# Kernel tuning notes

Measured on AMD Instinct MI355X. Metric: run time of the kernel, lower is better.

## Reference

```python
import jax, jax.numpy as jnp
import numpy as np

NUM_EMBEDDINGS = 8192
EMBEDDING_DIM = 512
COMMITMENT_COST = 0.25
EMA_DECAY = 0.99
EPS = 1e-5


def setup_inputs() -> dict:
    key = jax.random.key(0)
    k1, k2, k3, k4 = jax.random.split(key, 4)
    B = 32768
    z = jax.random.normal(k1, (B, EMBEDDING_DIM), dtype=jnp.float32)
    weight = jax.random.normal(k2, (NUM_EMBEDDINGS, EMBEDDING_DIM), dtype=jnp.float32)
    ema_cluster_size = jax.random.uniform(k3, (NUM_EMBEDDINGS,), dtype=jnp.float32)
    ema_dw = jax.random.normal(k4, (NUM_EMBEDDINGS, EMBEDDING_DIM), dtype=jnp.float32)
    return {"z": z, "weight": weight, "ema_cluster_size": ema_cluster_size, "ema_dw": ema_dw}


def reference(z, weight, ema_cluster_size, ema_dw):
    K = weight.shape[0]
    # Squared-L2 distances: (B, K) = |z|^2 + |e|^2 - 2 z e^T
    distances = (
        jnp.sum(z * z, axis=1, keepdims=True)
        + jnp.sum(weight * weight, axis=1)
        - 2.0 * (z @ weight.T)
    )
    indices = jnp.argmin(distances, axis=1)          # (B,)
    quantized_raw = weight[indices]                  # (B, D) gather

    # EMA codebook update (training-mode buffers; one-hot scatter-add == segment_sum)
    counts = jax.ops.segment_sum(jnp.ones(z.shape[0], dtype=z.dtype), indices, num_segments=K)
    dw = jax.ops.segment_sum(z, indices, num_segments=K)  # encodings.T @ z
    new_cluster_size = ema_cluster_size * EMA_DECAY + (1.0 - EMA_DECAY) * counts
    new_ema_dw = ema_dw * EMA_DECAY + (1.0 - EMA_DECAY) * dw
    n = jnp.sum(new_cluster_size)
    cluster_size = (new_cluster_size + EPS) / (n + K * EPS) * n
    new_weight = new_ema_dw / cluster_size[:, None]

    commitment_loss = COMMITMENT_COST * jnp.mean((z - jax.lax.stop_gradient(quantized_raw)) ** 2)
    quantized = z + jax.lax.stop_gradient(quantized_raw - z)  # straight-through
    return quantized, indices, commitment_loss, new_weight, new_cluster_size, new_ema_dw
```

## Files before the change

### kernel.cpp

```cpp
#include <hip/hip_runtime.h>

#define B_N 32768
#define D_N 512
#define K_N 8192
#define EMA 0.99f
#define ONE_M_EMA 0.01f
#define EPS_ 1e-5f
#define CCOST 0.25f

#define ZP_OFF 295936ull
#define WP_OFF 100959232ull
#define WS_NEED (WP_OFF + 25165824ull)
#define CNT_OFF    295936ull
#define OFFS_OFF   332800ull
#define CURS_OFF   365568ull
#define ROWL_OFF   398336ull
#define LPART_OFF  529408ull

typedef __attribute__((ext_vector_type(8))) short bf16x8;
typedef __attribute__((ext_vector_type(4))) float f32x4;

__global__ __launch_bounds__(256) void prep_kernel(const float* __restrict__ w,
                                                   const float* __restrict__ ecs,
                                                   float* __restrict__ wsq,
                                                   float* __restrict__ ncs_out) {
  int row  = blockIdx.x * 4 + (threadIdx.x >> 6);
  int lane = threadIdx.x & 63;
  const float* p = w + (size_t)row * D_N + lane * 8;
  float4 a = *(const float4*)p;
  float4 b = *(const float4*)(p + 4);
  float s = a.x*a.x + a.y*a.y + a.z*a.z + a.w*a.w
          + b.x*b.x + b.y*b.y + b.z*b.z + b.w*b.w;
  #pragma unroll
  for (int off = 32; off; off >>= 1) s += __shfl_down(s, off);
  if (lane == 0) wsq[row] = s;

  int gid = blockIdx.x * 256 + threadIdx.x;
  if (gid < K_N) ncs_out[gid] = EMA * ecs[gid];
}

__global__ __launch_bounds__(256) void prep_nedw(const float4* __restrict__ edw,
                                                 float4* __restrict__ nedw) {
  int i = blockIdx.x * 256 + threadIdx.x;
  float4 v = edw[i];
  v.x *= EMA; v.y *= EMA; v.z *= EMA; v.w *= EMA;
  nedw[i] = v;
}

__global__ __launch_bounds__(256) void split_pack(const float* __restrict__ x,
                                                  ushort* __restrict__ xp,
                                                  int R, int mode) {
  int g   = blockIdx.x * 256 + threadIdx.x;
  int row = g >> 6, c = g & 63;
  const float* src = x + (size_t)row * 512 + c * 8;
  float v[8];
  *(float4*)&v[0] = *(const float4*)&src[0];
  *(float4*)&v[4] = *(const float4*)&src[4];
  uint hw[4], lw[4];
  #pragma unroll
  for (int i = 0; i < 4; i++) {
    uint b0 = __float_as_uint(v[2*i]);
    uint b1 = __float_as_uint(v[2*i+1]);
    float r0 = v[2*i]   - __uint_as_float(b0 & 0xFFFF0000u);
    float r1 = v[2*i+1] - __uint_as_float(b1 & 0xFFFF0000u);
    hw[i] = (b0 >> 16) | (b1 & 0xFFFF0000u);
    lw[i] = (__float_as_uint(r0) >> 16) | (__float_as_uint(r1) & 0xFFFF0000u);
  }
  uint4 H = {hw[0], hw[1], hw[2], hw[3]};
  uint4 L = {lw[0], lw[1], lw[2], lw[3]};
  int si  = c >> 2;
  int p   = (c & 3) ^ ((row >> 1) & 3);
  size_t sstr = (size_t)R * 32;
  size_t base = (size_t)row * 32 + (size_t)p * 8;
  size_t d0 = (size_t)(si)      * sstr + base;
  size_t d1 = (size_t)(16 + si) * sstr + base;
  size_t d2 = (size_t)(32 + si) * sstr + base;
  if (mode == 0) { *(uint4*)&xp[d0] = H; *(uint4*)&xp[d1] = H; *(uint4*)&xp[d2] = L; }
  else           { *(uint4*)&xp[d0] = H; *(uint4*)&xp[d1] = L; *(uint4*)&xp[d2] = H; }
}

constexpr int COLT2 = 8;

#define GLDS(SRC, DST) __builtin_amdgcn_global_load_lds((const unsigned int*)(SRC), (unsigned int*)(DST), 16, 0, 0)

#define PHASE(AC, BC, AL, BL, G)                                               \
  {                                                                            \
    const int g_ = (G);                                                        \
    if (g_ + 1 <= 383) {                                                       \
      const char* Ab_ = (const char*)As[(g_ + 1) & 3] + aoff;                  \
      const char* Bb_ = (const char*)Bs[(g_ + 1) & 3] + boff;                  \
      _Pragma("unroll")                                                        \
      for (int i_ = 0; i_ < 8; i_++) AL[i_] = *(const bf16x8*)(Ab_ + i_ * 1024);\
      _Pragma("unroll")                                                        \
      for (int j_ = 0; j_ < 4; j_++) BL[j_] = *(const bf16x8*)(Bb_ + j_ * 1024);\
    }                                                                          \
    if (g_ + 4 <= 383) {                                                       \
      const int slotF_ = sf & 3;                                               \
      GLDS(zA + (size_t)sf * 2097152,        (char*)As[slotF_] + t * 16);      \
      GLDS(zA + (size_t)sf * 2097152 + 8192, (char*)As[slotF_] + 8192 + t * 16);\
      const size_t wOfs_ = (size_t)sf * 524288 + (size_t)ctf * 16384;          \
      GLDS(wB + wOfs_,        (char*)Bs[slotF_] + t * 16);                     \
      GLDS(wB + wOfs_ + 8192, (char*)Bs[slotF_] + 8192 + t * 16);              \
      sf++; if (sf == 48) { sf = 0; ctf++; }                                   \
    }                                                                          \
    __builtin_amdgcn_s_setprio(1);                                             \
    _Pragma("unroll")                                                          \
    for (int i_ = 0; i_ < 8; i_++)                                             \
      _Pragma("unroll")                                                        \
      for (int j_ = 0; j_ < 4; j_++)                                           \
        acc[i_][j_] = __builtin_amdgcn_mfma_f32_16x16x32_bf16(AC[i_], BC[j_],  \
                                                        acc[i_][j_], 0, 0, 0); \
    __builtin_amdgcn_s_setprio(0);                                             \
    asm volatile("s_waitcnt lgkmcnt(0)" ::: "memory");                         \
    if (g_ <= 379)      { asm volatile("s_waitcnt vmcnt(8)" ::: "memory"); }   \
    else if (g_ == 380) { asm volatile("s_waitcnt vmcnt(4)" ::: "memory"); }   \
    else if (g_ == 381) { asm volatile("s_waitcnt vmcnt(0)" ::: "memory"); }   \
    __builtin_amdgcn_s_barrier();                                              \
    __builtin_amdgcn_sched_barrier(0);                                         \
  }

__global__ __launch_bounds__(512, 2) void score3p(
    const ushort* __restrict__ zp, const ushort* __restrict__ wp,
    const float* __restrict__ wsq, unsigned long long* __restrict__ packed) {
  __shared__ ushort As[4][8192];
  __shared__ ushort Bs[4][8192];
  __shared__ float wsqs[2048];
  __shared__ unsigned long long best2[256][4];

  const int t = threadIdx.x, lane = t & 63, wid = t >> 6;
  const int wm = wid >> 2, wn = wid & 3;
  const int l15 = lane & 15, lg = (lane >> 4) & 3;
  const int row0 = blockIdx.x * 256;
  const int cg0  = blockIdx.y * 2048;

  const char* zA = (const char*)zp + ((size_t)(row0 + (t >> 2)) * 64 + (size_t)(t & 3) * 16);
  const char* wB = (const char*)wp + ((size_t)(cg0  + (t >> 2)) * 64 + (size_t)(t & 3) * 16);

  const int swz  = (l15 >> 1) & 3;
  const int aoff = (wm * 128 + l15) * 64 + ((lg ^ swz) * 16);
  const int boff = (wn * 64  + l15) * 64 + ((lg ^ swz) * 16);

  { float4 v = *(const float4*)&wsq[cg0 + t * 4]; *(float4*)&wsqs[t * 4] = v; }
  if (t < 256) { best2[t][0] = ~0ull; best2[t][1] = ~0ull; best2[t][2] = ~0ull; best2[t][3] = ~0ull; }
  __syncthreads();

  #pragma unroll
  for (int s0 = 0; s0 < 4; s0++) {
    GLDS(zA + (size_t)s0 * 2097152,        (char*)As[s0] + t * 16);
    GLDS(zA + (size_t)s0 * 2097152 + 8192, (char*)As[s0] + 8192 + t * 16);
    GLDS(wB + (size_t)s0 * 524288,         (char*)Bs[s0] + t * 16);
    GLDS(wB + (size_t)s0 * 524288 + 8192,  (char*)Bs[s0] + 8192 + t * 16);
  }
  asm volatile("s_waitcnt vmcnt(8)" ::: "memory");
  __builtin_amdgcn_s_barrier();
  __builtin_amdgcn_sched_barrier(0);

  bf16x8 aE[8], bE[4], aO[8], bO[4];
  #pragma unroll
  for (int i = 0; i < 8; i++) aE[i] = *(const bf16x8*)((const char*)As[0] + aoff + i * 1024);
  #pragma unroll
  for (int j = 0; j < 4; j++) bE[j] = *(const bf16x8*)((const char*)Bs[0] + boff + j * 1024);
  asm volatile("s_waitcnt lgkmcnt(0)" ::: "memory");
  __builtin_amdgcn_s_barrier();
  __builtin_amdgcn_sched_barrier(0);

  int sf = 4, ctf = 0;

  for (int ct = 0; ct < COLT2; ct++) {
    f32x4 acc[8][4];
    #pragma unroll
    for (int i = 0; i < 8; i++)
      #pragma unroll
      for (int j = 0; j < 4; j++) acc[i][j] = (f32x4){0.f, 0.f, 0.f, 0.f};

    for (int s = 0; s < 48; s += 2) {
      const int g = ct * 48 + s;
      PHASE(aE, bE, aO, bO, g)
      PHASE(aO, bO, aE, bE, g + 1)
    }

    float rv[32]; int rx[32];
    #pragma unroll
    for (int i = 0; i < 8; i++)
      #pragma unroll
      for (int r = 0; r < 4; r++) {
        float bvv = 3.4e38f; int bii = 0;
        #pragma unroll
        for (int j = 0; j < 4; j++) {
          float wq = wsqs[ct * 256 + wn * 64 + j * 16 + l15];
          float dist = wq - 2.0f * acc[i][j][r];
          int c = cg0 + ct * 256 + wn * 64 + j * 16 + l15;
          if (dist < bvv) { bvv = dist; bii = c; }
        }
        rv[i * 4 + r] = bvv; rx[i * 4 + r] = bii;
      }
    #pragma unroll
    for (int e = 0; e < 32; e++) {
      float v = rv[e]; int ix = rx[e];
      #pragma unroll
      for (int m = 1; m < 16; m <<= 1) {
        float ov = __shfl_xor(v, m, 64);
        int   oi = __shfl_xor(ix, m, 64);
        if (ov < v || (ov == v && oi < ix)) { v = ov; ix = oi; }
      }
      rv[e] = v; rx[e] = ix;
    }
    #pragma unroll
    for (int half = 0; half < 2; half++) {
      const int e0 = l15 + half * 16;
      float bvv = 0.f; int bii = 0;
      #pragma unroll
      for (int e = 0; e < 32; e++) {
        bool p = (e == e0);
        bvv = p ? rv[e] : bvv; bii = p ? rx[e] : bii;
      }
      unsigned u = __float_as_uint(bvv);
      u = (u & 0x80000000u) ? ~u : (u | 0x80000000u);
      unsigned long long key = ((unsigned long long)u << 32) | (unsigned)bii;
      const int rowl = wm * 128 + (e0 >> 2) * 16 + lg * 4 + (e0 & 3);
      unsigned long long cur = best2[rowl][wn];
      if (key < cur) best2[rowl][wn] = key;
    }
  }

  __syncthreads();
  if (t < 256) {
    unsigned long long k0 = best2[t][0], k1 = best2[t][1];
    unsigned long long k2 = best2[t][2], k3 = best2[t][3];
    unsigned long long m0 = k0 < k1 ? k0 : k1;
    unsigned long long m1 = k2 < k3 ? k2 : k3;
    atomicMin(&packed[row0 + t], m0 < m1 ? m0 : m1);
  }
}

constexpr int LDP = 40;
constexpr int KSPLIT = 8, COLT = K_N / KSPLIT / 128;
__device__ __forceinline__ void stage16(const float* __restrict__ g,
                                        ushort* __restrict__ h,
                                        ushort* __restrict__ l) {
  float v[16];
  *(float4*)&v[0]  = *(const float4*)&g[0];
  *(float4*)&v[4]  = *(const float4*)&g[4];
  *(float4*)&v[8]  = *(const float4*)&g[8];
  *(float4*)&v[12] = *(const float4*)&g[12];
  uint hw[8], lw[8];
  #pragma unroll
  for (int i = 0; i < 8; i++) {
    uint b0 = __float_as_uint(v[2*i]);
    uint b1 = __float_as_uint(v[2*i+1]);
    float r0 = v[2*i]   - __uint_as_float(b0 & 0xFFFF0000u);
    float r1 = v[2*i+1] - __uint_as_float(b1 & 0xFFFF0000u);
    hw[i] = (b0 >> 16) | (b1 & 0xFFFF0000u);
    lw[i] = (__float_as_uint(r0) >> 16) | (__float_as_uint(r1) & 0xFFFF0000u);
  }
  ((uint4*)h)[0] = *(uint4*)&hw[0];
  ((uint4*)h)[1] = *(uint4*)&hw[4];
  ((uint4*)l)[0] = *(uint4*)&lw[0];
  ((uint4*)l)[1] = *(uint4*)&lw[4];
}

__global__ __launch_bounds__(256, 2) void score_argmin_mfma(
    const float* __restrict__ z, const float* __restrict__ w,
    const float* __restrict__ wsq, unsigned long long* __restrict__ packed) {
  __shared__ ushort Ah[128][LDP];
  __shared__ ushort Al[128][LDP];
  __shared__ ushort Bh[128][LDP];
  __shared__ ushort Bl[128][LDP];
  const int t = threadIdx.x, lane = t & 63, wid = t >> 6;
  const int wm = wid >> 1, wn = wid & 1;
  const int l15 = lane & 15, lg = lane >> 4;
  const int row0 = blockIdx.x * 128;
  const int ks0  = blockIdx.y * (K_N / KSPLIT);
  const int srow = t >> 1, skq = (t & 1) * 16;
  float rmin[16]; int ridx[16];
  #pragma unroll
  for (int e = 0; e < 16; e++) { rmin[e] = 3.4e38f; ridx[e] = 0; }
  for (int ct = 0; ct < COLT; ct++) {
    const int c0 = ks0 + ct * 128;
    f32x4 acc[4][4];
    #pragma unroll
    for (int i = 0; i < 4; i++)
      #pragma unroll
      for (int j = 0; j < 4; j++) acc[i][j] = (f32x4){0.f, 0.f, 0.f, 0.f};
    for (int k0 = 0; k0 < D_N; k0 += 32) {
      __syncthreads();
      stage16(&z[(size_t)(row0 + srow) * D_N + k0 + skq], &Ah[srow][skq], &Al[srow][skq]);
      stage16(&w[(size_t)(c0   + srow) * D_N + k0 + skq], &Bh[srow][skq], &Bl[srow][skq]);
      __syncthreads();
      bf16x8 ah[4], al[4], bh[4], bl[4];
      #pragma unroll
      for (int i = 0; i < 4; i++) {
        ah[i] = *(const bf16x8*)&Ah[wm*64 + i*16 + l15][lg*8];
        al[i] = *(const bf16x8*)&Al[wm*64 + i*16 + l15][lg*8];
        bh[i] = *(const bf16x8*)&Bh[wn*64 + i*16 + l15][lg*8];
        bl[i] = *(const bf16x8*)&Bl[wn*64 + i*16 + l15][lg*8];
      }
      #pragma unroll
      for (int i = 0; i < 4; i++)
        #pragma unroll
        for (int j = 0; j < 4; j++) {
          acc[i][j] = __builtin_amdgcn_mfma_f32_16x16x32_bf16(ah[i], bh[j], acc[i][j], 0, 0, 0);
          acc[i][j] = __builtin_amdgcn_mfma_f32_16x16x32_bf16(ah[i], bl[j], acc[i][j], 0, 0, 0);
          acc[i][j] = __builtin_amdgcn_mfma_f32_16x16x32_bf16(al[i], bh[j], acc[i][j], 0, 0, 0);
        }
    }
    float wq[4];
    #pragma unroll
    for (int j = 0; j < 4; j++) wq[j] = wsq[c0 + wn*64 + j*16 + l15];
    #pragma unroll
    for (int i = 0; i < 4; i++)
      #pragma unroll
      for (int r = 0; r < 4; r++) {
        const int e = i * 4 + r;
        #pragma unroll
        for (int j = 0; j < 4; j++) {
          float dist = wq[j] - 2.0f * acc[i][j][r];
          if (dist < rmin[e]) { rmin[e] = dist; ridx[e] = c0 + wn*64 + j*16 + l15; }
        }
      }
  }
  #pragma unroll
  for (int e = 0; e < 16; e++) {
    float v = rmin[e]; int ix = ridx[e];
    #pragma unroll
    for (int m = 1; m < 16; m <<= 1) {
      float ov = __shfl_xor(v, m, 64);
      int   oi = __shfl_xor(ix, m, 64);
      if (ov < v || (ov == v && oi < ix)) { v = ov; ix = oi; }
    }
    rmin[e] = v; ridx[e] = ix;
  }
  const int s = l15;
  float bv = 0.f; int bi = 0;
  #pragma unroll
  for (int e = 0; e < 16; e++) {
    bool p = (e == s);
    bv = p ? rmin[e] : bv;
    bi = p ? ridx[e] : bi;
  }
  unsigned u = __float_as_uint(bv);
  u = (u & 0x80000000u) ? ~u : (u | 0x80000000u);
  unsigned long long key = ((unsigned long long)u << 32) | (unsigned)bi;
  atomicMin(&packed[row0 + wm*64 + (s >> 2)*16 + lg*4 + (s & 3)], key);
}

__global__ __launch_bounds__(256) void count_kernel(
    const unsigned long long* __restrict__ packed, int* __restrict__ cnt,
    float* __restrict__ idxout) {
  int row = blockIdx.x * 256 + threadIdx.x;
  int idx = (int)(packed[row] & 0xFFFFFFFFull);
  idxout[row] = (float)idx;
  atomicAdd(&cnt[idx], 1);
}

__global__ __launch_bounds__(256) void scan_kernel(const int* __restrict__ cnt,
                                                   int* __restrict__ offs,
                                                   int* __restrict__ cursor) {
  int t = threadIdx.x;
  int base = t * 32;
  int local[32];
  int s = 0;
  #pragma unroll
  for (int i = 0; i < 32; i++) { local[i] = s; s += cnt[base + i]; }
  __shared__ int ps[257];
  ps[t + 1] = s;
  if (t == 0) ps[0] = 0;
  __syncthreads();
  if (t == 0) { for (int i = 1; i <= 256; i++) ps[i] += ps[i - 1]; }
  __syncthreads();
  int e = ps[t];
  #pragma unroll
  for (int i = 0; i < 32; i++) {
    int o = e + local[i];
    offs[base + i] = o; cursor[base + i] = o;
  }
  if (t == 255) offs[8192] = ps[256];
}

__global__ __launch_bounds__(256) void scatter_ids(
    const unsigned long long* __restrict__ packed, int* __restrict__ cursor,
    int* __restrict__ rowlist) {
  int row = blockIdx.x * 256 + threadIdx.x;
  int idx = (int)(packed[row] & 0xFFFFFFFFull);
  int pos = atomicAdd(&cursor[idx], 1);
  rowlist[pos] = row;
}

__global__ __launch_bounds__(256) void seg_accum(
    const float* __restrict__ z, const float* __restrict__ edw,
    const float* __restrict__ ecs, const int* __restrict__ offs,
    const int* __restrict__ rowlist, float* __restrict__ nedw_out,
    float* __restrict__ ncs_out) {
  int k = blockIdx.x, t = threadIdx.x;
  int s0 = offs[k], s1 = offs[k + 1];
  float ax = 0.f, ay = 0.f;
  for (int r = s0; r < s1; r++) {
    int row = rowlist[r];
    float2 zv = *(const float2*)&z[(size_t)row * D_N + t * 2];
    ax += zv.x; ay += zv.y;
  }
  float2 ev = *(const float2*)&edw[(size_t)k * D_N + t * 2];
  float2 o;
  o.x = EMA * ev.x + ONE_M_EMA * ax;
  o.y = EMA * ev.y + ONE_M_EMA * ay;
  *(float2*)&nedw_out[(size_t)k * D_N + t * 2] = o;
  if (t == 0) ncs_out[k] = EMA * ecs[k] + ONE_M_EMA * (float)(s1 - s0);
}

__global__ __launch_bounds__(256) void quant_loss(
    const float* __restrict__ z, const float* __restrict__ w,
    const unsigned long long* __restrict__ packed,
    float* __restrict__ qout, float* __restrict__ lpart) {
  int row = blockIdx.x, t = threadIdx.x;
  int idx = (int)(packed[row] & 0xFFFFFFFFull);
  float2 zv = *(const float2*)&z[(size_t)row * D_N + t * 2];
  float2 wv = *(const float2*)&w[(size_t)idx * D_N + t * 2];
  float2 q;
  q.x = zv.x + (wv.x - zv.x);
  q.y = zv.y + (wv.y - zv.y);
  *(float2*)&qout[(size_t)row * D_N + t * 2] = q;
  float dx = zv.x - wv.x, dy = zv.y - wv.y;
  float s = dx * dx + dy * dy;
  #pragma unroll
  for (int off = 32; off; off >>= 1) s += __shfl_down(s, off);
  __shared__ float part[4];
  if ((t & 63) == 0) part[t >> 6] = s;
  __syncthreads();
  if (t == 0) lpart[row] = part[0] + part[1] + part[2] + part[3];
}

__global__ __launch_bounds__(256) void reduce2(const float* __restrict__ ncs_out,
                                               const float* __restrict__ lpart,
                                               float* __restrict__ nsum,
                                               float* __restrict__ loss_sum) {
  int t = threadIdx.x;
  float s1 = 0.f, s2 = 0.f;
  for (int i = t; i < K_N; i += 256) s1 += ncs_out[i];
  for (int i = t; i < B_N; i += 256) s2 += lpart[i];
  #pragma unroll
  for (int off = 32; off; off >>= 1) {
    s1 += __shfl_down(s1, off);
    s2 += __shfl_down(s2, off);
  }
  __shared__ float p1[4], p2[4];
  if ((t & 63) == 0) { p1[t >> 6] = s1; p2[t >> 6] = s2; }
  __syncthreads();
  if (t == 0) {
    nsum[0]     = p1[0] + p1[1] + p1[2] + p1[3];
    loss_sum[0] = p2[0] + p2[1] + p2[2] + p2[3];
  }
}

__global__ __launch_bounds__(256) void gather_scatter(
    const float* __restrict__ z, const float* __restrict__ w,
    const unsigned long long* __restrict__ packed,
    float* __restrict__ qout, float* __restrict__ idxout,
    float* __restrict__ ncs_out, float* __restrict__ nedw_out,
    float* __restrict__ loss_sum) {
  int row = blockIdx.x;
  int t   = threadIdx.x;
  int idx = (int)(packed[row] & 0xFFFFFFFFull);
  float2 zv = *(const float2*)&z[(size_t)row * D_N + t * 2];
  float2 wv = *(const float2*)&w[(size_t)idx * D_N + t * 2];
  float2 q;
  q.x = zv.x + (wv.x - zv.x);
  q.y = zv.y + (wv.y - zv.y);
  *(float2*)&qout[(size_t)row * D_N + t * 2] = q;
  float dx = zv.x - wv.x, dy = zv.y - wv.y;
  float s = dx*dx + dy*dy;
  #pragma unroll
  for (int off = 32; off; off >>= 1) s += __shfl_down(s, off);
  __shared__ float part[4];
  if ((t & 63) == 0) part[t >> 6] = s;
  __syncthreads();
  if (t == 0) {
    atomicAdd(loss_sum, part[0] + part[1] + part[2] + part[3]);
    atomicAdd(&ncs_out[idx], ONE_M_EMA);
    idxout[row] = (float)idx;
  }
  atomicAdd(&nedw_out[(size_t)idx * D_N + t*2],     ONE_M_EMA * zv.x);
  atomicAdd(&nedw_out[(size_t)idx * D_N + t*2 + 1], ONE_M_EMA * zv.y);
}

__global__ __launch_bounds__(256) void reduce_n(const float* __restrict__ ncs_out,
                                                float* __restrict__ nsum) {
  int t = threadIdx.x;
  float s = 0.f;
  for (int i = t; i < K_N; i += 256) s += ncs_out[i];
  #pragma unroll
  for (int off = 32; off; off >>= 1) s += __shfl_down(s, off);
  __shared__ float part[4];
  if ((t & 63) == 0) part[t >> 6] = s;
  __syncthreads();
  if (t == 0) nsum[0] = part[0] + part[1] + part[2] + part[3];
}

__global__ __launch_bounds__(256) void finalize(
    const float* __restrict__ ncs_out, const float* __restrict__ nedw_out,
    float* __restrict__ nw_out, const float* __restrict__ nsum,
    const float* __restrict__ loss_sum, float* __restrict__ loss_out) {
  size_t i = (size_t)blockIdx.x * 256 + threadIdx.x;
  float n = nsum[0];
  int k = (int)(i >> 9);
  float nv = ncs_out[k];
  float cs = (nv + EPS_) / (n + K_N * EPS_) * n;
  nw_out[i] = nedw_out[i] / cs;
  if (i == 0) loss_out[0] = CCOST * loss_sum[0] / (float)((size_t)B_N * D_N);
}

extern "C" void kernel_launch(void* const* d_in, const int* in_sizes, int n_in,
                              void* d_out, int out_size, void* d_ws, size_t ws_size,
                              hipStream_t stream) {
  const float* z   = (const float*)d_in[0];
  const float* w   = (const float*)d_in[1];
  const float* ecs = (const float*)d_in[2];
  const float* edw = (const float*)d_in[3];

  float* out      = (float*)d_out;
  float* qout     = out;
  float* idxout   = out + (size_t)B_N * D_N;
  float* loss_out = idxout + B_N;
  float* nw_out   = loss_out + 1;
  float* ncs_out  = nw_out + (size_t)K_N * D_N;
  float* nedw_out = ncs_out + K_N;

  unsigned long long* packed = (unsigned long long*)d_ws;
  float* wsq      = (float*)((char*)d_ws + 262144);
  float* loss_sum = (float*)((char*)d_ws + 294912);
  float* nsum     = loss_sum + 1;

  hipMemsetAsync(d_ws, 0xFF, 262144, stream);
  hipMemsetAsync((void*)loss_sum, 0, 8, stream);

  prep_kernel<<<2048, 256, 0, stream>>>(w, ecs, wsq, ncs_out);

  if (ws_size >= WS_NEED) {
    ushort* zp  = (ushort*)((char*)d_ws + ZP_OFF);
    ushort* wp  = (ushort*)((char*)d_ws + WP_OFF);
    int* cnt    = (int*)((char*)d_ws + CNT_OFF);
    int* offs   = (int*)((char*)d_ws + OFFS_OFF);
    int* cursor = (int*)((char*)d_ws + CURS_OFF);
    int* rowl   = (int*)((char*)d_ws + ROWL_OFF);
    float* lpart= (float*)((char*)d_ws + LPART_OFF);

    split_pack<<<8192, 256, 0, stream>>>(z, zp, B_N, 0);
    split_pack<<<2048, 256, 0, stream>>>(w, wp, K_N, 1);
    score3p<<<dim3(128, 4), 512, 0, stream>>>(zp, wp, wsq, packed);
    hipMemsetAsync((void*)cnt, 0, K_N * sizeof(int), stream);
    count_kernel<<<B_N / 256, 256, 0, stream>>>(packed, cnt, idxout);
    scan_kernel<<<1, 256, 0, stream>>>(cnt, offs, cursor);
    scatter_ids<<<B_N / 256, 256, 0, stream>>>(packed, cursor, rowl);
    seg_accum<<<K_N, 256, 0, stream>>>(z, edw, ecs, offs, rowl, nedw_out, ncs_out);
    quant_loss<<<B_N, 256, 0, stream>>>(z, w, packed, qout, lpart);
    reduce2<<<1, 256, 0, stream>>>(ncs_out, lpart, nsum, loss_sum);
  } else {
    prep_nedw<<<4096, 256, 0, stream>>>((const float4*)edw, (float4*)nedw_out);
    score_argmin_mfma<<<dim3(B_N / 128, KSPLIT), 256, 0, stream>>>(z, w, wsq, packed);
    gather_scatter<<<B_N, 256, 0, stream>>>(z, w, packed, qout, idxout,
                                            ncs_out, nedw_out, loss_sum);
    reduce_n<<<1, 256, 0, stream>>>(ncs_out, nsum);
  }

  finalize<<<K_N * D_N / 256, 256, 0, stream>>>(ncs_out, nedw_out, nw_out,
                                                nsum, loss_sum, loss_out);
}
```

Measured before the change: 1.029 ms.

## Score with single bf16 pass and refine ambiguous rows with exact fp32 distances

Replaces the three-pass split-bf16 score GEMM (hi*hi, hi*lo, lo*hi) with a single hi*hi bf16 pass. Each tile keeps its best and second-best candidate, and a fixup kernel uses a Cauchy-Schwarz error bound on the dropped terms to accept rows whose winner is clearly separated. The remaining rows are queued and re-scored in fp32 over their candidate columns. This cuts GEMM work to about a third, at the cost of extra kernels, a large per-row candidate buffer, and refine work that depends on how many rows turn out ambiguous.

```diff
diff --git a/kernel.cpp b/kernel.cpp
--- a/kernel.cpp
+++ b/kernel.cpp
@@ -8,9 +8,14 @@
 #define EPS_ 1e-5f
 #define CCOST 0.25f
 
-#define ZP_OFF 295936ull
-#define WP_OFF 100959232ull
-#define WS_NEED (WP_OFF + 25165824ull)
+#define ZP_OFF    295936ull
+#define WP_OFF    33850368ull
+#define DIST_OFF  42238976ull
+#define THR_OFF   109347840ull
+#define ZH2_OFF   109478912ull
+#define ZL2_OFF   109609984ull
+#define QROWS_OFF 109741056ull
+#define WS_NEED   109872128ull
 #define CNT_OFF    295936ull
 #define OFFS_OFF   332800ull
 #define CURS_OFF   365568ull
@@ -47,36 +52,67 @@
   nedw[i] = v;
 }
 
-__global__ __launch_bounds__(256) void split_pack(const float* __restrict__ x,
-                                                  ushort* __restrict__ xp,
-                                                  int R, int mode) {
-  int g   = blockIdx.x * 256 + threadIdx.x;
+__global__ __launch_bounds__(256) void split_z(const float* __restrict__ x,
+                                               ushort* __restrict__ xp,
+                                               float* __restrict__ zh2,
+                                               float* __restrict__ zl2) {
+  int g = blockIdx.x * 256 + threadIdx.x;
   int row = g >> 6, c = g & 63;
   const float* src = x + (size_t)row * 512 + c * 8;
   float v[8];
   *(float4*)&v[0] = *(const float4*)&src[0];
   *(float4*)&v[4] = *(const float4*)&src[4];
-  uint hw[4], lw[4];
+  uint hw[4]; float h2 = 0.f, l2 = 0.f;
   #pragma unroll
   for (int i = 0; i < 4; i++) {
     uint b0 = __float_as_uint(v[2*i]);
     uint b1 = __float_as_uint(v[2*i+1]);
-    float r0 = v[2*i]   - __uint_as_float(b0 & 0xFFFF0000u);
-    float r1 = v[2*i+1] - __uint_as_float(b1 & 0xFFFF0000u);
+    float h0 = __uint_as_float(b0 & 0xFFFF0000u);
+    float h1 = __uint_as_float(b1 & 0xFFFF0000u);
+    float r0 = v[2*i] - h0, r1 = v[2*i+1] - h1;
     hw[i] = (b0 >> 16) | (b1 & 0xFFFF0000u);
-    lw[i] = (__float_as_uint(r0) >> 16) | (__float_as_uint(r1) & 0xFFFF0000u);
-  }
-  uint4 H = {hw[0], hw[1], hw[2], hw[3]};
-  uint4 L = {lw[0], lw[1], lw[2], lw[3]};
-  int si  = c >> 2;
-  int p   = (c & 3) ^ ((row >> 1) & 3);
-  size_t sstr = (size_t)R * 32;
-  size_t base = (size_t)row * 32 + (size_t)p * 8;
-  size_t d0 = (size_t)(si)      * sstr + base;
-  size_t d1 = (size_t)(16 + si) * sstr + base;
-  size_t d2 = (size_t)(32 + si) * sstr + base;
-  if (mode == 0) { *(uint4*)&xp[d0] = H; *(uint4*)&xp[d1] = H; *(uint4*)&xp[d2] = L; }
-  else           { *(uint4*)&xp[d0] = H; *(uint4*)&xp[d1] = L; *(uint4*)&xp[d2] = H; }
+    h2 += h0*h0 + h1*h1;  l2 += r0*r0 + r1*r1;
+  }
+  int si = c >> 2;
+  int p  = (c & 3) ^ ((row >> 1) & 3);
+  size_t d0 = (size_t)si * (32768u * 32u) + (size_t)row * 32 + (size_t)p * 8;
+  *(uint4*)&xp[d0] = (uint4){hw[0], hw[1], hw[2], hw[3]};
+  #pragma unroll
+  for (int off = 32; off; off >>= 1) { h2 += __shfl_down(h2, off); l2 += __shfl_down(l2, off); }
+  if (c == 0) { zh2[row] = h2; zl2[row] = l2; }
+}
+
+__global__ __launch_bounds__(256) void split_w(const float* __restrict__ x,
+                                               ushort* __restrict__ xp,
+                                               unsigned* __restrict__ maxwl2,
+                                               unsigned* __restrict__ maxw2) {
+  int g = blockIdx.x * 256 + threadIdx.x;
+  int row = g >> 6, c = g & 63;
+  const float* src = x + (size_t)row * 512 + c * 8;
+  float v[8];
+  *(float4*)&v[0] = *(const float4*)&src[0];
+  *(float4*)&v[4] = *(const float4*)&src[4];
+  uint hw[4]; float w2 = 0.f, l2 = 0.f;
+  #pragma unroll
+  for (int i = 0; i < 4; i++) {
+    uint b0 = __float_as_uint(v[2*i]);
+    uint b1 = __float_as_uint(v[2*i+1]);
+    float h0 = __uint_as_float(b0 & 0xFFFF0000u);
+    float h1 = __uint_as_float(b1 & 0xFFFF0000u);
+    float r0 = v[2*i] - h0, r1 = v[2*i+1] - h1;
+    hw[i] = (b0 >> 16) | (b1 & 0xFFFF0000u);
+    w2 += v[2*i]*v[2*i] + v[2*i+1]*v[2*i+1];  l2 += r0*r0 + r1*r1;
+  }
+  int si = c >> 2;
+  int p  = (c & 3) ^ ((row >> 1) & 3);
+  size_t d0 = (size_t)si * (8192u * 32u) + (size_t)row * 32 + (size_t)p * 8;
+  *(uint4*)&xp[d0] = (uint4){hw[0], hw[1], hw[2], hw[3]};
+  #pragma unroll
+  for (int off = 32; off; off >>= 1) { w2 += __shfl_down(w2, off); l2 += __shfl_down(l2, off); }
+  if (c == 0) {
+    atomicMax(maxwl2, __float_as_uint(l2));
+    atomicMax(maxw2,  __float_as_uint(w2));
+  }
 }
 
 constexpr int COLT2 = 8;
@@ -86,7 +122,7 @@
 #define PHASE(AC, BC, AL, BL, G)                                               \
   {                                                                            \
     const int g_ = (G);                                                        \
-    if (g_ + 1 <= 383) {                                                       \
+    if (g_ + 1 <= 127) {                                                       \
       const char* Ab_ = (const char*)As[(g_ + 1) & 3] + aoff;                  \
       const char* Bb_ = (const char*)Bs[(g_ + 1) & 3] + boff;                  \
       _Pragma("unroll")                                                        \
@@ -94,14 +130,14 @@
       _Pragma("unroll")                                                        \
       for (int j_ = 0; j_ < 4; j_++) BL[j_] = *(const bf16x8*)(Bb_ + j_ * 1024);\
     }                                                                          \
-    if (g_ + 4 <= 383) {                                                       \
+    if (g_ + 4 <= 127) {                                                       \
       const int slotF_ = sf & 3;                                               \
       GLDS(zA + (size_t)sf * 2097152,        (char*)As[slotF_] + t * 16);      \
       GLDS(zA + (size_t)sf * 2097152 + 8192, (char*)As[slotF_] + 8192 + t * 16);\
       const size_t wOfs_ = (size_t)sf * 524288 + (size_t)ctf * 16384;          \
       GLDS(wB + wOfs_,        (char*)Bs[slotF_] + t * 16);                     \
       GLDS(wB + wOfs_ + 8192, (char*)Bs[slotF_] + 8192 + t * 16);              \
-      sf++; if (sf == 48) { sf = 0; ctf++; }                                   \
+      sf++; if (sf == 16) { sf = 0; ctf++; }                                   \
     }                                                                          \
     __builtin_amdgcn_s_setprio(1);                                             \
     _Pragma("unroll")                                                          \
@@ -112,20 +148,19 @@
                                                         acc[i_][j_], 0, 0, 0); \
     __builtin_amdgcn_s_setprio(0);                                             \
     asm volatile("s_waitcnt lgkmcnt(0)" ::: "memory");                         \
-    if (g_ <= 379)      { asm volatile("s_waitcnt vmcnt(8)" ::: "memory"); }   \
-    else if (g_ == 380) { asm volatile("s_waitcnt vmcnt(4)" ::: "memory"); }   \
-    else if (g_ == 381) { asm volatile("s_waitcnt vmcnt(0)" ::: "memory"); }   \
+    if (g_ <= 123)      { asm volatile("s_waitcnt vmcnt(8)" ::: "memory"); }   \
+    else if (g_ == 124) { asm volatile("s_waitcnt vmcnt(4)" ::: "memory"); }   \
+    else if (g_ == 125) { asm volatile("s_waitcnt vmcnt(0)" ::: "memory"); }   \
     __builtin_amdgcn_s_barrier();                                              \
     __builtin_amdgcn_sched_barrier(0);                                         \
   }
 
-__global__ __launch_bounds__(512, 2) void score3p(
+__global__ __launch_bounds__(512, 2) void score_h(
     const ushort* __restrict__ zp, const ushort* __restrict__ wp,
-    const float* __restrict__ wsq, unsigned long long* __restrict__ packed) {
+    const float* __restrict__ wsq, float4* __restrict__ dist12) {
   __shared__ ushort As[4][8192];
   __shared__ ushort Bs[4][8192];
   __shared__ float wsqs[2048];
-  __shared__ unsigned long long best2[256][4];
 
   const int t = threadIdx.x, lane = t & 63, wid = t >> 6;
   const int wm = wid >> 2, wn = wid & 3;
@@ -141,7 +176,6 @@
   const int boff = (wn * 64  + l15) * 64 + ((lg ^ swz) * 16);
 
   { float4 v = *(const float4*)&wsq[cg0 + t * 4]; *(float4*)&wsqs[t * 4] = v; }
-  if (t < 256) { best2[t][0] = ~0ull; best2[t][1] = ~0ull; best2[t][2] = ~0ull; best2[t][3] = ~0ull; }
   __syncthreads();
 
   #pragma unroll
@@ -173,63 +207,157 @@
       #pragma unroll
       for (int j = 0; j < 4; j++) acc[i][j] = (f32x4){0.f, 0.f, 0.f, 0.f};
 
-    for (int s = 0; s < 48; s += 2) {
-      const int g = ct * 48 + s;
+    for (int s = 0; s < 16; s += 2) {
+      const int g = ct * 16 + s;
       PHASE(aE, bE, aO, bO, g)
       PHASE(aO, bO, aE, bE, g + 1)
     }
 
-    float rv[32]; int rx[32];
+    const int tileG = blockIdx.y * 8 + ct;
     #pragma unroll
-    for (int i = 0; i < 8; i++)
+    for (int ch = 0; ch < 4; ch++) {
+      float v1[8], v2[8]; int i1[8];
       #pragma unroll
-      for (int r = 0; r < 4; r++) {
-        float bvv = 3.4e38f; int bii = 0;
+      for (int u = 0; u < 8; u++) {
+        const int i = 2 * ch + (u >> 2), r = u & 3;
+        float b1 = 3.4e38f, b2 = 3.4e38f; int bi = 0x7FFFFFFF;
         #pragma unroll
         for (int j = 0; j < 4; j++) {
           float wq = wsqs[ct * 256 + wn * 64 + j * 16 + l15];
-          float dist = wq - 2.0f * acc[i][j][r];
-          int c = cg0 + ct * 256 + wn * 64 + j * 16 + l15;
-          if (dist < bvv) { bvv = dist; bii = c; }
+          float d  = wq - 2.0f * acc[i][j][r];
+          int cc   = cg0 + ct * 256 + wn * 64 + j * 16 + l15;
+          if (d < b1)      { b2 = b1; b1 = d; bi = cc; }
+          else if (d < b2) { b2 = d; }
         }
-        rv[i * 4 + r] = bvv; rx[i * 4 + r] = bii;
+        v1[u] = b1; i1[u] = bi; v2[u] = b2;
       }
-    #pragma unroll
-    for (int e = 0; e < 32; e++) {
-      float v = rv[e]; int ix = rx[e];
       #pragma unroll
-      for (int m = 1; m < 16; m <<= 1) {
-        float ov = __shfl_xor(v, m, 64);
-        int   oi = __shfl_xor(ix, m, 64);
-        if (ov < v || (ov == v && oi < ix)) { v = ov; ix = oi; }
+      for (int u = 0; u < 8; u++) {
+        float a1 = v1[u], a2 = v2[u]; int ai = i1[u];
+        #pragma unroll
+        for (int m = 1; m < 16; m <<= 1) {
+          float o1 = __shfl_xor(a1, m, 64);
+          int   oi = __shfl_xor(ai, m, 64);
+          float o2 = __shfl_xor(a2, m, 64);
+          bool tb = (o1 < a1) || (o1 == a1 && oi < ai);
+          float lose = tb ? a1 : o1;
+          a2 = fminf(fminf(a2, o2), lose);
+          a1 = tb ? o1 : a1; ai = tb ? oi : ai;
+        }
+        v1[u] = a1; i1[u] = ai; v2[u] = a2;
       }
-      rv[e] = v; rx[e] = ix;
+      const int wbase = (ch & 1) * 8;
+      if (l15 >= wbase && l15 < wbase + 8) {
+        const int eu = l15 - wbase;
+        float f1 = 0.f, f2 = 0.f; int fi = 0;
+        #pragma unroll
+        for (int u = 0; u < 8; u++) {
+          bool p = (u == eu);
+          f1 = p ? v1[u] : f1; fi = p ? i1[u] : fi; f2 = p ? v2[u] : f2;
+        }
+        const int e = 8 * ch + eu;
+        const int rowG = row0 + wm * 128 + (e >> 2) * 16 + lg * 4 + (e & 3);
+        float4 st; st.x = f1; st.y = __int_as_float(fi); st.z = f2; st.w = 0.f;
+        dist12[(size_t)rowG * 128 + tileG * 4 + wn] = st;
+      }
     }
+  }
+}
+
+__global__ __launch_bounds__(256) void fixup_kernel(
+    const float4* __restrict__ dist12, const float* __restrict__ zh2,
+    const float* __restrict__ zl2, const float* __restrict__ scal,
+    unsigned long long* __restrict__ packed, float* __restrict__ thresh_arr,
+    int* __restrict__ qrows, int* __restrict__ qcount) {
+  int row  = blockIdx.x * 4 + (threadIdx.x >> 6);
+  int lane = threadIdx.x & 63;
+  const float4* base = dist12 + (size_t)row * 128;
+  float4 ea = base[lane];
+  float4 eb = base[lane + 64];
+  float v1, v2; int i1;
+  {
+    bool tb = (eb.x < ea.x) || (eb.x == ea.x && __float_as_int(eb.y) < __float_as_int(ea.y));
+    float lose = tb ? ea.x : eb.x;
+    v2 = fminf(fminf(ea.z, eb.z), lose);
+    v1 = tb ? eb.x : ea.x;
+    i1 = __float_as_int(tb ? eb.y : ea.y);
+  }
+  #pragma unroll
+  for (int m = 1; m < 64; m <<= 1) {
+    float o1 = __shfl_xor(v1, m, 64);
+    int   oi = __shfl_xor(i1, m, 64);
+    float o2 = __shfl_xor(v2, m, 64);
+    bool tb = (o1 < v1) || (o1 == v1 && oi < i1);
+    float lose = tb ? v1 : o1;
+    v2 = fminf(fminf(v2, o2), lose);
+    v1 = tb ? o1 : v1; i1 = tb ? oi : i1;
+  }
+  if (lane == 0) {
+    float B = 2.0f * (sqrtf(zh2[row]) * sqrtf(scal[2]) + sqrtf(zl2[row]) * sqrtf(scal[3]));
+    float thr = v1 + 2.05f * B + 1e-5f;
+    if (v2 > thr) {
+      packed[row] = (unsigned long long)(unsigned)i1;
+    } else {
+      thresh_arr[row] = thr;
+      int p = atomicAdd(qcount, 1);
+      qrows[p] = row;
+    }
+  }
+}
+
+__device__ __forceinline__ float exact_dist(const float* __restrict__ w,
+                                            const float* __restrict__ wsq,
+                                            float4 za, float4 zb, int ki, int lane) {
+  const float* wr = w + (size_t)ki * 512 + lane * 8;
+  float4 wa = *(const float4*)wr;
+  float4 wb = *(const float4*)(wr + 4);
+  float s = za.x*wa.x + za.y*wa.y + za.z*wa.z + za.w*wa.w
+          + zb.x*wb.x + zb.y*wb.y + zb.z*wb.z + zb.w*wb.w;
+  #pragma unroll
+  for (int m = 1; m < 64; m <<= 1) s += __shfl_xor(s, m, 64);
+  return wsq[ki] - 2.0f * s;
+}
+
+__global__ __launch_bounds__(256) void refine_kernel(
+    const float* __restrict__ z, const float* __restrict__ w,
+    const float* __restrict__ wsq, const float4* __restrict__ dist12,
+    const float* __restrict__ thresh_arr, const int* __restrict__ qrows,
+    const int* __restrict__ qcount, unsigned long long* __restrict__ packed) {
+  int wgid = (blockIdx.x * 256 + threadIdx.x) >> 6;
+  int lane = threadIdx.x & 63;
+  int n  = qcount[0];
+  int nw = gridDim.x * 4;
+  for (int it = wgid; it < n; it += nw) {
+    int row = qrows[it];
+    float thr = thresh_arr[row];
+    const float* zr = z + (size_t)row * 512 + lane * 8;
+    float4 za = *(const float4*)zr;
+    float4 zb = *(const float4*)(zr + 4);
+    const float4* base = dist12 + (size_t)row * 128;
+    float bestd = 3.4e38f; int besti = 0x7FFFFFFF;
     #pragma unroll
     for (int half = 0; half < 2; half++) {
-      const int e0 = l15 + half * 16;
-      float bvv = 0.f; int bii = 0;
-      #pragma unroll
-      for (int e = 0; e < 32; e++) {
-        bool p = (e == e0);
-        bvv = p ? rv[e] : bvv; bii = p ? rx[e] : bii;
+      float4 e = base[lane + half * 64];
+      unsigned long long mc = __ballot(e.x <= thr);
+      unsigned long long ms = __ballot(e.z <= thr);
+      while (mc) {
+        int src = __ffsll(mc) - 1; mc &= mc - 1;
+        int ki = __shfl(__float_as_int(e.y), src);
+        float d = exact_dist(w, wsq, za, zb, ki, lane);
+        if (d < bestd || (d == bestd && ki < besti)) { bestd = d; besti = ki; }
       }
-      unsigned u = __float_as_uint(bvv);
-      u = (u & 0x80000000u) ? ~u : (u | 0x80000000u);
-      unsigned long long key = ((unsigned long long)u << 32) | (unsigned)bii;
-      const int rowl = wm * 128 + (e0 >> 2) * 16 + lg * 4 + (e0 & 3);
-      unsigned long long cur = best2[rowl][wn];
-      if (key < cur) best2[rowl][wn] = key;
+      while (ms) {
+        int src = __ffsll(ms) - 1; ms &= ms - 1;
+        int g2 = src + half * 64;
+        int col0 = (g2 >> 2) * 256 + (g2 & 3) * 64;
+        for (int q = 0; q < 64; q++) {
+          int ki = col0 + q;
+          float d = exact_dist(w, wsq, za, zb, ki, lane);
+          if (d < bestd || (d == bestd && ki < besti)) { bestd = d; besti = ki; }
+        }
+      }
     }
-  }
-
-  __syncthreads();
-  if (t < 256) {
-    unsigned long long k0 = best2[t][0], k1 = best2[t][1];
-    unsigned long long k2 = best2[t][2], k3 = best2[t][3];
-    unsigned long long m0 = k0 < k1 ? k0 : k1;
-    unsigned long long m1 = k2 < k3 ? k2 : k3;
-    atomicMin(&packed[row0 + t], m0 < m1 ? m0 : m1);
+    if (lane == 0) packed[row] = (unsigned long long)(unsigned)besti;
   }
 }
 
@@ -526,26 +654,36 @@
 
   unsigned long long* packed = (unsigned long long*)d_ws;
   float* wsq      = (float*)((char*)d_ws + 262144);
-  float* loss_sum = (float*)((char*)d_ws + 294912);
-  float* nsum     = loss_sum + 1;
+  float* scal     = (float*)((char*)d_ws + 294912);
+  float* loss_sum = scal;
+  float* nsum     = scal + 1;
 
   hipMemsetAsync(d_ws, 0xFF, 262144, stream);
-  hipMemsetAsync((void*)loss_sum, 0, 8, stream);
+  hipMemsetAsync((void*)scal, 0, 20, stream);
 
   prep_kernel<<<2048, 256, 0, stream>>>(w, ecs, wsq, ncs_out);
 
   if (ws_size >= WS_NEED) {
-    ushort* zp  = (ushort*)((char*)d_ws + ZP_OFF);
-    ushort* wp  = (ushort*)((char*)d_ws + WP_OFF);
+    ushort* zp   = (ushort*)((char*)d_ws + ZP_OFF);
+    ushort* wp   = (ushort*)((char*)d_ws + WP_OFF);
+    float4* d12  = (float4*)((char*)d_ws + DIST_OFF);
+    float* thra  = (float*)((char*)d_ws + THR_OFF);
+    float* zh2   = (float*)((char*)d_ws + ZH2_OFF);
+    float* zl2   = (float*)((char*)d_ws + ZL2_OFF);
+    int*   qrows = (int*)((char*)d_ws + QROWS_OFF);
     int* cnt    = (int*)((char*)d_ws + CNT_OFF);
     int* offs   = (int*)((char*)d_ws + OFFS_OFF);
     int* cursor = (int*)((char*)d_ws + CURS_OFF);
     int* rowl   = (int*)((char*)d_ws + ROWL_OFF);
     float* lpart= (float*)((char*)d_ws + LPART_OFF);
 
-    split_pack<<<8192, 256, 0, stream>>>(z, zp, B_N, 0);
-    split_pack<<<2048, 256, 0, stream>>>(w, wp, K_N, 1);
-    score3p<<<dim3(128, 4), 512, 0, stream>>>(zp, wp, wsq, packed);
+    split_z<<<8192, 256, 0, stream>>>(z, zp, zh2, zl2);
+    split_w<<<2048, 256, 0, stream>>>(w, wp, (unsigned*)&scal[2], (unsigned*)&scal[3]);
+    score_h<<<dim3(128, 4), 512, 0, stream>>>(zp, wp, wsq, d12);
+    fixup_kernel<<<8192, 256, 0, stream>>>(d12, zh2, zl2, scal, packed, thra,
+                                           qrows, (int*)&scal[4]);
+    refine_kernel<<<512, 256, 0, stream>>>(z, w, wsq, d12, thra, qrows,
+                                           (const int*)&scal[4], packed);
     hipMemsetAsync((void*)cnt, 0, K_N * sizeof(int), stream);
     count_kernel<<<B_N / 256, 256, 0, stream>>>(packed, cnt, idxout);
     scan_kernel<<<1, 256, 0, stream>>>(cnt, offs, cursor);
```

Result: slower. 2.081 ms (+102.2%).

## Restructure score GEMM main loop into half-slice LDS reads with 3-deep prefetch

Applied to the files above, without the earlier changes.

Replaces the double-buffered register pipeline (full A/B fragments for the next slice preloaded while computing the current one) with a per-slice schedule. Each slice is split into two halves: it reads half of the A fragments plus all B from LDS, issues the async global-to-LDS loads, runs 16 MFMAs, then repeats for the second half. The global prefetch depth drops from 4 slices to 3. The aim is to cut register pressure (no duplicated aE/aO/bE/bO sets) and interleave LDS reads with MFMA work. The cost is extra barriers per slice and less latency hiding, since LDS reads now sit on the critical path before each MFMA group.

```diff
diff --git a/kernel.cpp b/kernel.cpp
--- a/kernel.cpp
+++ b/kernel.cpp
@@ -80,46 +80,69 @@
 }
 
 constexpr int COLT2 = 8;
+constexpr int NSLICE = 384;
 
 #define GLDS(SRC, DST) __builtin_amdgcn_global_load_lds((const unsigned int*)(SRC), (unsigned int*)(DST), 16, 0, 0)
 
-#define PHASE(AC, BC, AL, BL, G)                                               \
+#define SLICE(G)                                                               \
   {                                                                            \
     const int g_ = (G);                                                        \
-    if (g_ + 1 <= 383) {                                                       \
-      const char* Ab_ = (const char*)As[(g_ + 1) & 3] + aoff;                  \
-      const char* Bb_ = (const char*)Bs[(g_ + 1) & 3] + boff;                  \
+    const char* Ab_ = (const char*)As[g_ & 3] + aoff;                          \
+    const char* Bb_ = (const char*)Bs[g_ & 3] + boff;                          \
+    bf16x8 af_[4], b_[4];                                                      \
+                           \
+    _Pragma("unroll")                                                          \
+    for (int i_ = 0; i_ < 4; i_++) af_[i_] = *(const bf16x8*)(Ab_ + i_ * 1024);\
+    _Pragma("unroll")                                                          \
+    for (int j_ = 0; j_ < 4; j_++) b_[j_]  = *(const bf16x8*)(Bb_ + j_ * 1024);\
+    if (g_ + 3 < NSLICE) {                                                     \
+      const int sl_ = (g_ + 3) & 3;                                            \
+      GLDS(zA + (size_t)sf * 2097152,        (char*)As[sl_] + t * 16);         \
+      GLDS(zA + (size_t)sf * 2097152 + 8192, (char*)As[sl_] + 8192 + t * 16);  \
+    }                                                                          \
+    __builtin_amdgcn_s_barrier();                                              \
+    asm volatile("s_waitcnt lgkmcnt(0)" ::: "memory");                         \
+    __builtin_amdgcn_sched_barrier(0);                                         \
+    __builtin_amdgcn_s_setprio(1);                                             \
+    _Pragma("unroll")                                                          \
+    for (int i_ = 0; i_ < 4; i_++)                                             \
       _Pragma("unroll")                                                        \
-      for (int i_ = 0; i_ < 8; i_++) AL[i_] = *(const bf16x8*)(Ab_ + i_ * 1024);\
-      _Pragma("unroll")                                                        \
-      for (int j_ = 0; j_ < 4; j_++) BL[j_] = *(const bf16x8*)(Bb_ + j_ * 1024);\
-    }                                                                          \
-    if (g_ + 4 <= 383) {                                                       \
-      const int slotF_ = sf & 3;                                               \
-      GLDS(zA + (size_t)sf * 2097152,        (char*)As[slotF_] + t * 16);      \
-      GLDS(zA + (size_t)sf * 2097152 + 8192, (char*)As[slotF_] + 8192 + t * 16);\
+      for (int j_ = 0; j_ < 4; j_++)                                           \
+        acc[i_][j_] = __builtin_amdgcn_mfma_f32_16x16x32_bf16(af_[i_], b_[j_], \
+                                                        acc[i_][j_], 0, 0, 0); \
+    __builtin_amdgcn_s_setprio(0);                                             \
+    __builtin_amdgcn_s_barrier();                                              \
+    __builtin_amdgcn_sched_barrier(0);                                         \
+                                      \
+    _Pragma("unroll")                                                          \
+    for (int i_ = 0; i_ < 4; i_++)                                             \
+      af_[i_] = *(const bf16x8*)(Ab_ + 4096 + i_ * 1024);                      \
+    if (g_ + 3 < NSLICE) {                                                     \
+      const int sl_ = (g_ + 3) & 3;                                            \
       const size_t wOfs_ = (size_t)sf * 524288 + (size_t)ctf * 16384;          \
-      GLDS(wB + wOfs_,        (char*)Bs[slotF_] + t * 16);                     \
-      GLDS(wB + wOfs_ + 8192, (char*)Bs[slotF_] + 8192 + t * 16);              \
+      GLDS(wB + wOfs_,        (char*)Bs[sl_] + t * 16);                        \
+      GLDS(wB + wOfs_ + 8192, (char*)Bs[sl_] + 8192 + t * 16);                 \
       sf++; if (sf == 48) { sf = 0; ctf++; }                                   \
     }                                                                          \
+    __builtin_amdgcn_s_barrier();                                              \
+    asm volatile("s_waitcnt lgkmcnt(0)" ::: "memory");                         \
+    __builtin_amdgcn_sched_barrier(0);                                         \
     __builtin_amdgcn_s_setprio(1);                                             \
     _Pragma("unroll")                                                          \
-    for (int i_ = 0; i_ < 8; i_++)                                             \
+    for (int i_ = 0; i_ < 4; i_++)                                             \
       _Pragma("unroll")                                                        \
       for (int j_ = 0; j_ < 4; j_++)                                           \
-        acc[i_][j_] = __builtin_amdgcn_mfma_f32_16x16x32_bf16(AC[i_], BC[j_],  \
-                                                        acc[i_][j_], 0, 0, 0); \
+        acc[4 + i_][j_] = __builtin_amdgcn_mfma_f32_16x16x32_bf16(af_[i_],     \
+                                          b_[j_], acc[4 + i_][j_], 0, 0, 0);   \
     __builtin_amdgcn_s_setprio(0);                                             \
-    asm volatile("s_waitcnt lgkmcnt(0)" ::: "memory");                         \
-    if (g_ <= 379)      { asm volatile("s_waitcnt vmcnt(8)" ::: "memory"); }   \
-    else if (g_ == 380) { asm volatile("s_waitcnt vmcnt(4)" ::: "memory"); }   \
-    else if (g_ == 381) { asm volatile("s_waitcnt vmcnt(0)" ::: "memory"); }   \
+    if (g_ <= NSLICE - 4)      { asm volatile("s_waitcnt vmcnt(8)" ::: "memory"); } \
+    else if (g_ == NSLICE - 3) { asm volatile("s_waitcnt vmcnt(4)" ::: "memory"); } \
+    else if (g_ == NSLICE - 2) { asm volatile("s_waitcnt vmcnt(0)" ::: "memory"); } \
     __builtin_amdgcn_s_barrier();                                              \
     __builtin_amdgcn_sched_barrier(0);                                         \
   }
 
-__global__ __launch_bounds__(512, 2) void score3p(
+__global__ __launch_bounds__(512, 2) void score3q(
     const ushort* __restrict__ zp, const ushort* __restrict__ wp,
     const float* __restrict__ wsq, unsigned long long* __restrict__ packed) {
   __shared__ ushort As[4][8192];
@@ -145,7 +168,7 @@
   __syncthreads();
 
   #pragma unroll
-  for (int s0 = 0; s0 < 4; s0++) {
+  for (int s0 = 0; s0 < 3; s0++) {
     GLDS(zA + (size_t)s0 * 2097152,        (char*)As[s0] + t * 16);
     GLDS(zA + (size_t)s0 * 2097152 + 8192, (char*)As[s0] + 8192 + t * 16);
     GLDS(wB + (size_t)s0 * 524288,         (char*)Bs[s0] + t * 16);
@@ -155,16 +178,7 @@
   __builtin_amdgcn_s_barrier();
   __builtin_amdgcn_sched_barrier(0);
 
-  bf16x8 aE[8], bE[4], aO[8], bO[4];
-  #pragma unroll
-  for (int i = 0; i < 8; i++) aE[i] = *(const bf16x8*)((const char*)As[0] + aoff + i * 1024);
-  #pragma unroll
-  for (int j = 0; j < 4; j++) bE[j] = *(const bf16x8*)((const char*)Bs[0] + boff + j * 1024);
-  asm volatile("s_waitcnt lgkmcnt(0)" ::: "memory");
-  __builtin_amdgcn_s_barrier();
-  __builtin_amdgcn_sched_barrier(0);
-
-  int sf = 4, ctf = 0;
+  int sf = 3, ctf = 0;
 
   for (int ct = 0; ct < COLT2; ct++) {
     f32x4 acc[8][4];
@@ -173,10 +187,9 @@
       #pragma unroll
       for (int j = 0; j < 4; j++) acc[i][j] = (f32x4){0.f, 0.f, 0.f, 0.f};
 
-    for (int s = 0; s < 48; s += 2) {
-      const int g = ct * 48 + s;
-      PHASE(aE, bE, aO, bO, g)
-      PHASE(aO, bO, aE, bE, g + 1)
+    #pragma unroll 4
+    for (int s = 0; s < 48; s++) {
+      SLICE(ct * 48 + s)
     }
 
     float rv[32]; int rx[32];
@@ -545,7 +558,7 @@
 
     split_pack<<<8192, 256, 0, stream>>>(z, zp, B_N, 0);
     split_pack<<<2048, 256, 0, stream>>>(w, wp, K_N, 1);
-    score3p<<<dim3(128, 4), 512, 0, stream>>>(zp, wp, wsq, packed);
+    score3q<<<dim3(128, 4), 512, 0, stream>>>(zp, wp, wsq, packed);
     hipMemsetAsync((void*)cnt, 0, K_N * sizeof(int), stream);
     count_kernel<<<B_N / 256, 256, 0, stream>>>(packed, cnt, idxout);
     scan_kernel<<<1, 256, 0, stream>>>(cnt, offs, cursor);
```

After: 1.103 ms. +7.1%, slower.
